# Optimization experiments

Measured on AMD Instinct MI355X. Metric: run time of the kernel, lower is better.

## Reference

```python
import jax, jax.numpy as jnp
import numpy as np

A_DIM = 12      # action dim (half of augmented state)
N_STEPS = 10    # Heun ODE steps (Flow.N)
P = 0.95        # mixing coefficient in _Heun_method


def _mlp(x, obs, t, W1, b1, W2, b2, W3, b3, W4, b4):
    h = jnp.concatenate([x, obs, t], axis=-1)
    h = jnp.tanh(h @ W1 + b1)
    h = jnp.tanh(h @ W2 + b2)
    h = jnp.tanh(h @ W3 + b3)
    return h @ W4 + b4


def _heun(obs, x, params):
    # Flow._Heun_method: sequential Heun integration of the augmented state.
    z = x[..., :A_DIM]
    y = x[..., A_DIM:]
    dt = 1.0 / N_STEPS
    tshape = x.shape[:-1] + (1,)

    def step(carry, i):
        z, y = carry
        t = jnp.ones(tshape, x.dtype) * (i / N_STEPS)
        z_t = _mlp(y, obs, t, *params)
        z_in = z + z_t * dt
        y_t = _mlp(z_in, obs, t, *params)
        y_in = y + y_t * dt
        z_new = P * z_in + (1.0 - P) * y_in
        y_new = P * y_in + (1.0 - P) * z_new
        return (z_new, y_new), None

    (z, y), _ = jax.lax.scan(step, (z, y), jnp.arange(N_STEPS, dtype=x.dtype))
    return jnp.concatenate([z, y], axis=-1)


def setup_inputs() -> dict:
    key = jax.random.key(0)
    ks = jax.random.split(key, 8)
    B, OBS, H, A = 2048, 48, 256, A_DIM
    din = A + OBS + 1  # 61
    s = 0.05  # small init scale to keep tanh unsaturated
    return {
        "observations": jax.random.normal(ks[0], (B, OBS), jnp.float32),
        "action_aug_0": jax.random.normal(ks[1], (B, 2 * A), jnp.float32),
        "W1": s * jax.random.normal(ks[2], (din, H), jnp.float32),
        "b1": jnp.zeros((H,), jnp.float32),
        "W2": s * jax.random.normal(ks[3], (H, H), jnp.float32),
        "b2": jnp.zeros((H,), jnp.float32),
        "W3": s * jax.random.normal(ks[4], (H, H), jnp.float32),
        "b3": jnp.zeros((H,), jnp.float32),
        "W4": s * jax.random.normal(ks[5], (H, A), jnp.float32),
        "b4": jnp.zeros((A,), jnp.float32),
        "jac": 1,
    }


def reference(observations, action_aug_0, W1, b1, W2, b2, W3, b3, W4, b4, jac):
    params = (W1, b1, W2, b2, W3, b3, W4, b4)
    action_aug = _heun(observations, action_aug_0, params)
    d = action_aug_0.shape[-1]
    # Normal(0, I) log prob summed over dims
    log_probs = -0.5 * jnp.sum(action_aug_0 ** 2, axis=-1) - 0.5 * d * jnp.log(2.0 * jnp.pi)
    if jac:
        single = lambda o, x: _heun(o, x, params)  # per-sample (obs_dim,), (2a,)
        J = jax.vmap(jax.jacrev(single, argnums=1))(observations, action_aug_0)  # (B, 2a, 2a)
        _, logabsdet = jnp.linalg.slogdet(J)  # = log|det J|
        log_probs = log_probs - logabsdet
    return action_aug, log_probs
```

## Files before the change

kernel.cpp:

```cpp
#include <hip/hip_runtime.h>
#include <hip/hip_bf16.h>


typedef unsigned short ushort_t;
typedef float f32x4 __attribute__((ext_vector_type(4)));
typedef short s16x8 __attribute__((ext_vector_type(8)));
typedef int   i32x4 __attribute__((ext_vector_type(4)));

#define NB      2048
#define OBS_D   48
#define HDIM    256
#define ADIM    12
#define XDIM    24
#define NSTEPS  10
#define DT      0.1f
#define PP      0.95f

#define W1U 0
#define W2U 16384
#define W3U 81920
#define W4U 147456
#define N_FRAG 151552
#define FRAG_BLOCKS 592
#define LP_BLOCKS 8

#define LDS_W2   0
#define LDS_BUFA 131072
#define LDS_BUFB 139264
#define LDS_AIN  147456
#define LDS_Z    149504
#define LDS_Y    150528
#define LDS_ZI   151552
#define LDS_TOTAL 152576

__device__ __forceinline__ ushort_t f2bf(float f) {
  unsigned u = __builtin_bit_cast(unsigned, f);
  u += 0x7fffu + ((u >> 16) & 1u);
  return (ushort_t)(u >> 16);
}

__device__ __forceinline__ float tanh_fast(float x) {
  float e = __builtin_amdgcn_exp2f(x * 2.885390081777927f);
  return 1.f - 2.f * __builtin_amdgcn_rcpf(1.f + e);
}

__global__ void prep_kernel(const float* __restrict__ W1, const float* __restrict__ b1,
                            const float* __restrict__ W2, const float* __restrict__ W3,
                            const float* __restrict__ W4, const float* __restrict__ x0,
                            const int* __restrict__ jac, float* __restrict__ out,
                            ushort_t* __restrict__ ws) {
  int bid = blockIdx.x;
  int tid = threadIdx.x;
  if (bid < FRAG_BLOCKS) {
    int e = bid * 256 + tid;
    float val = 0.f;
    if (e < 16384) {
      int kt = e >> 13; int r = e & 8191;
      int nt = r >> 9, l = (r >> 3) & 63, j = r & 7;
      int k = kt * 32 + ((l >> 4) << 3) + j;
      int col = nt * 16 + (l & 15);
      val = (k < 61) ? W1[k * 256 + col] : ((k == 61) ? b1[col] : 0.f);
    } else if (e < 81920) {
      int e2 = e - 16384;
      int kt = e2 >> 13; int r = e2 & 8191;
      int nt = r >> 9, l = (r >> 3) & 63, j = r & 7;
      int k = kt * 32 + ((l >> 4) << 3) + j;
      int col = nt * 16 + (l & 15);
      val = W2[k * 256 + col];
    } else if (e < 147456) {
      int e2 = e - 81920;
      int kt = e2 >> 13; int r = e2 & 8191;
      int nt = r >> 9, l = (r >> 3) & 63, j = r & 7;
      int k = kt * 32 + ((l >> 4) << 3) + j;
      int col = nt * 16 + (l & 15);
      val = W3[k * 256 + col];
    } else {
      int e2 = e - 147456;
      int kt = e2 >> 9; int r = e2 & 511;
      int l = (r >> 3) & 63, j = r & 7;
      int k = kt * 32 + ((l >> 4) << 3) + j;
      int col = l & 15;
      val = (col < 12) ? W4[k * 12 + col] : 0.f;
    }
    ws[e] = f2bf(val);
  } else {
    int s = (bid - FRAG_BLOCKS) * 256 + tid;
    float acc = 0.f;
    #pragma unroll 4
    for (int j = 0; j < XDIM; ++j) { float v = x0[s * XDIM + j]; acc += v * v; }
    float C = (jac[0] != 0) ? -9.744134143900015f : -22.054524796912143f;
    out[NB * XDIM + s] = -0.5f * acc + C;
  }
}

__global__ __launch_bounds__(512, 2) void flow_main(
    const float* __restrict__ obs, const float* __restrict__ x0,
    const float* __restrict__ b2g, const float* __restrict__ b3g,
    const float* __restrict__ b4g, const ushort_t* __restrict__ ws,
    float* __restrict__ out) {
  extern __shared__ char lds[];
  const int tid  = threadIdx.x;
  const int lane = tid & 63;
  const int wv   = tid >> 6;
  const int g    = lane >> 4;
  const int ar   = lane & 15;
  const int row0 = blockIdx.x * 16;

  ((unsigned*)(lds + LDS_AIN))[tid] = 0u;

  {
    const i32x4* __restrict__ src = (const i32x4*)(ws + W2U);
    i32x4* dst = (i32x4*)(lds + LDS_W2);
    #pragma unroll
    for (int it = 0; it < 16; ++it) dst[it * 512 + tid] = src[it * 512 + tid];
  }
  __syncthreads();

  for (int idx = tid; idx < 16 * OBS_D; idx += 512) {
    int r = idx / OBS_D, o = idx - r * OBS_D;
    int k = 12 + o;
    float v = obs[(row0 + r) * OBS_D + o];
    int byt = (k * 2) ^ ((r & 7) << 4);
    *(ushort_t*)(lds + LDS_AIN + r * 128 + byt) = f2bf(v);
  }
  if (tid < 16) {
    int byt = (61 * 2) ^ ((tid & 7) << 4);
    *(ushort_t*)(lds + LDS_AIN + tid * 128 + byt) = (ushort_t)0x3F80;
  }
  if (tid < 192) {
    int r = tid / 12, d = tid - r * 12;
    float zv = x0[(row0 + r) * XDIM + d];
    float yv = x0[(row0 + r) * XDIM + 12 + d];
    ((float*)(lds + LDS_Z))[r * 16 + d] = zv;
    ((float*)(lds + LDS_Y))[r * 16 + d] = yv;
    int byt = (d * 2) ^ ((r & 7) << 4);
    *(ushort_t*)(lds + LDS_AIN + r * 128 + byt) = f2bf(yv);
  }

  s16x8 w1r[2][2], w3r[8][2], w4r;
  #pragma unroll
  for (int kt = 0; kt < 2; ++kt)
    #pragma unroll
    for (int n = 0; n < 2; ++n)
      w1r[kt][n] = *(const s16x8*)(ws + W1U + (((kt * 16) + (2 * wv + n)) * 64 + lane) * 8);
  #pragma unroll
  for (int kt = 0; kt < 8; ++kt)
    #pragma unroll
    for (int n = 0; n < 2; ++n)
      w3r[kt][n] = *(const s16x8*)(ws + W3U + (((kt * 16) + (2 * wv + n)) * 64 + lane) * 8);
  w4r = *(const s16x8*)(ws + W4U + (wv * 64 + lane) * 8);

  float b2r[2], b3r[2];
  #pragma unroll
  for (int n = 0; n < 2; ++n) {
    b2r[n] = b2g[(2 * wv + n) * 16 + ar];
    b3r[n] = b3g[(2 * wv + n) * 16 + ar];
  }
  float b4v = (ar < 12) ? b4g[ar] : 0.f;

  __syncthreads();

  const f32x4 z4 = {0.f, 0.f, 0.f, 0.f};

  for (int i = 0; i < NSTEPS; ++i) {
    #pragma unroll
    for (int ev = 0; ev < 2; ++ev) {
      f32x4 acc0 = z4, acc1 = z4;
      #pragma unroll
      for (int kt = 0; kt < 2; ++kt) {
        int off = kt * 64 + g * 16;
        s16x8 a = *(const s16x8*)(lds + LDS_AIN + ar * 128 + (off ^ ((ar & 7) << 4)));
        acc0 = __builtin_amdgcn_mfma_f32_16x16x32_bf16(a, w1r[kt][0], acc0, 0, 0, 0);
        acc1 = __builtin_amdgcn_mfma_f32_16x16x32_bf16(a, w1r[kt][1], acc1, 0, 0, 0);
      }
      #pragma unroll
      for (int n = 0; n < 2; ++n) {
        f32x4 acc = n ? acc1 : acc0;
        int colg = (2 * wv + n) * 16 + ar;
        #pragma unroll
        for (int r = 0; r < 4; ++r) {
          int rw = g * 4 + r;
          float h = tanh_fast(acc[r]);
          int byt = (colg * 2) ^ ((rw & 7) << 4);
          *(ushort_t*)(lds + LDS_BUFA + rw * 512 + byt) = f2bf(h);
        }
      }
      __syncthreads();

      acc0 = z4; acc1 = z4;
      #pragma unroll
      for (int kt = 0; kt < 8; ++kt) {
        int off = kt * 64 + g * 16;
        s16x8 a = *(const s16x8*)(lds + LDS_BUFA + ar * 512 + (off ^ ((ar & 7) << 4)));
        s16x8 bb0 = *(const s16x8*)(lds + LDS_W2 + (((kt * 16) + (2 * wv)) * 64 + lane) * 16);
        s16x8 bb1 = *(const s16x8*)(lds + LDS_W2 + (((kt * 16) + (2 * wv + 1)) * 64 + lane) * 16);
        acc0 = __builtin_amdgcn_mfma_f32_16x16x32_bf16(a, bb0, acc0, 0, 0, 0);
        acc1 = __builtin_amdgcn_mfma_f32_16x16x32_bf16(a, bb1, acc1, 0, 0, 0);
      }
      #pragma unroll
      for (int n = 0; n < 2; ++n) {
        f32x4 acc = n ? acc1 : acc0;
        int colg = (2 * wv + n) * 16 + ar;
        #pragma unroll
        for (int r = 0; r < 4; ++r) {
          int rw = g * 4 + r;
          float h = tanh_fast(acc[r] + b2r[n]);
          int byt = (colg * 2) ^ ((rw & 7) << 4);
          *(ushort_t*)(lds + LDS_BUFB + rw * 512 + byt) = f2bf(h);
        }
      }
      __syncthreads();

      acc0 = z4; acc1 = z4;
      #pragma unroll
      for (int kt = 0; kt < 8; ++kt) {
        int off = kt * 64 + g * 16;
        s16x8 a = *(const s16x8*)(lds + LDS_BUFB + ar * 512 + (off ^ ((ar & 7) << 4)));
        acc0 = __builtin_amdgcn_mfma_f32_16x16x32_bf16(a, w3r[kt][0], acc0, 0, 0, 0);
        acc1 = __builtin_amdgcn_mfma_f32_16x16x32_bf16(a, w3r[kt][1], acc1, 0, 0, 0);
      }
      #pragma unroll
      for (int n = 0; n < 2; ++n) {
        f32x4 acc = n ? acc1 : acc0;
        int colg = (2 * wv + n) * 16 + ar;
        #pragma unroll
        for (int r = 0; r < 4; ++r) {
          int rw = g * 4 + r;
          float h = tanh_fast(acc[r] + b3r[n]);
          int byt = (colg * 2) ^ ((rw & 7) << 4);
          *(ushort_t*)(lds + LDS_BUFA + rw * 512 + byt) = f2bf(h);
        }
      }
      __syncthreads();

      {
        int off = wv * 64 + g * 16;
        s16x8 a = *(const s16x8*)(lds + LDS_BUFA + ar * 512 + (off ^ ((ar & 7) << 4)));
        f32x4 p = __builtin_amdgcn_mfma_f32_16x16x32_bf16(a, w4r, z4, 0, 0, 0);
        #pragma unroll
        for (int r = 0; r < 4; ++r) {
          int rw = g * 4 + r;
          *(float*)(lds + LDS_BUFB + wv * 1024 + (rw * 16 + ar) * 4) = p[r];
        }
      }
      __syncthreads();

      if (tid < 256) {
        float s = b4v;
        #pragma unroll
        for (int w = 0; w < 8; ++w) s += *(const float*)(lds + LDS_BUFB + w * 1024 + tid * 4);
        int r = tid >> 4, c = tid & 15;
        if (c < 12) {
          int byt = (c * 2) ^ ((r & 7) << 4);
          if (ev == 0) {
            float zi = ((float*)(lds + LDS_Z))[tid] + DT * s;
            ((float*)(lds + LDS_ZI))[tid] = zi;
            *(ushort_t*)(lds + LDS_AIN + r * 128 + byt) = f2bf(zi);
          } else {
            float yi = ((float*)(lds + LDS_Y))[tid] + DT * s;
            float zi = ((float*)(lds + LDS_ZI))[tid];
            float zn = PP * zi + (1.f - PP) * yi;
            float yn = PP * yi + (1.f - PP) * zn;
            ((float*)(lds + LDS_Z))[tid] = zn;
            ((float*)(lds + LDS_Y))[tid] = yn;
            *(ushort_t*)(lds + LDS_AIN + r * 128 + byt) = f2bf(yn);
          }
        }
        if (ev == 1 && c == 15) {
          float tn = (float)(i + 1) * DT;
          int byt = (60 * 2) ^ ((r & 7) << 4);
          *(ushort_t*)(lds + LDS_AIN + r * 128 + byt) = f2bf(tn);
        }
      }
      __syncthreads();
    }
  }

  if (tid < 256) {
    int r = tid >> 4, c = tid & 15;
    if (c < 12) {
      out[(row0 + r) * XDIM + c]      = ((float*)(lds + LDS_Z))[tid];
      out[(row0 + r) * XDIM + 12 + c] = ((float*)(lds + LDS_Y))[tid];
    }
  }
}

extern "C" void kernel_launch(void* const* d_in, const int* in_sizes, int n_in,
                              void* d_out, int out_size, void* d_ws, size_t ws_size,
                              hipStream_t stream) {
  const float* obs = (const float*)d_in[0];
  const float* x0  = (const float*)d_in[1];
  const float* W1  = (const float*)d_in[2];
  const float* b1  = (const float*)d_in[3];
  const float* W2  = (const float*)d_in[4];
  const float* b2  = (const float*)d_in[5];
  const float* W3  = (const float*)d_in[6];
  const float* b3  = (const float*)d_in[7];
  const float* W4  = (const float*)d_in[8];
  const float* b4  = (const float*)d_in[9];
  const int*   jac = (const int*)d_in[10];
  float* out = (float*)d_out;
  ushort_t* ws = (ushort_t*)d_ws;

  hipFuncSetAttribute((const void*)flow_main,
                      hipFuncAttributeMaxDynamicSharedMemorySize, LDS_TOTAL);

  prep_kernel<<<FRAG_BLOCKS + LP_BLOCKS, 256, 0, stream>>>(W1, b1, W2, W3, W4, x0, jac, out, ws);
  flow_main<<<128, 512, LDS_TOTAL, stream>>>(obs, x0, b2, b3, b4, ws, out);
}
```

Baseline: 56.55 us.

## Keep W2 in registers, repack LDS activation layout, drop a barrier

W2 fragments are now held in registers like W3 instead of being staged in a 128KB LDS buffer, which removes the LDS copy at kernel start and the per-step W2 LDS reads. The weight fragment K ordering and the activation LDS layout are permuted so each lane writes packed 32-bit pairs with padded row strides instead of XOR-swizzled 16-bit stores. The barrier before the final layer is replaced by a local lgkmcnt wait, since each wave reads only the columns it wrote itself. z/y state is kept in registers instead of LDS. The cost is much higher register pressure, which may spill under launch_bounds(512,2).

```diff
diff --git a/kernel.cpp b/kernel.cpp
--- a/kernel.cpp
+++ b/kernel.cpp
@@ -5,7 +5,6 @@
 typedef unsigned short ushort_t;
 typedef float f32x4 __attribute__((ext_vector_type(4)));
 typedef short s16x8 __attribute__((ext_vector_type(8)));
-typedef int   i32x4 __attribute__((ext_vector_type(4)));
 
 #define NB      2048
 #define OBS_D   48
@@ -24,14 +23,11 @@
 #define FRAG_BLOCKS 592
 #define LP_BLOCKS 8
 
-#define LDS_W2   0
-#define LDS_BUFA 131072
-#define LDS_BUFB 139264
-#define LDS_AIN  147456
-#define LDS_Z    149504
-#define LDS_Y    150528
-#define LDS_ZI   151552
-#define LDS_TOTAL 152576
+#define LDS_BUFA 0
+#define LDS_BUFB 9216
+#define LDS_AIN  18432
+#define LDS_PART 21504
+#define LDS_TOTAL 31744
 
 __device__ __forceinline__ ushort_t f2bf(float f) {
   unsigned u = __builtin_bit_cast(unsigned, f);
@@ -42,6 +38,10 @@
 __device__ __forceinline__ float tanh_fast(float x) {
   float e = __builtin_amdgcn_exp2f(x * 2.885390081777927f);
   return 1.f - 2.f * __builtin_amdgcn_rcpf(1.f + e);
+}
+
+__device__ __forceinline__ int ain_byte(int r, int c) {
+  return r * 192 + ((c >> 5) << 6) + ((c & 15) << 2) + (((c >> 4) & 1) << 1);
 }
 
 __global__ void prep_kernel(const float* __restrict__ W1, const float* __restrict__ b1,
@@ -57,28 +57,28 @@
     if (e < 16384) {
       int kt = e >> 13; int r = e & 8191;
       int nt = r >> 9, l = (r >> 3) & 63, j = r & 7;
-      int k = kt * 32 + ((l >> 4) << 3) + j;
+      int k = kt * 32 + ((l >> 4) << 2) + (j >> 1) + ((j & 1) << 4);
       int col = nt * 16 + (l & 15);
       val = (k < 61) ? W1[k * 256 + col] : ((k == 61) ? b1[col] : 0.f);
     } else if (e < 81920) {
       int e2 = e - 16384;
       int kt = e2 >> 13; int r = e2 & 8191;
       int nt = r >> 9, l = (r >> 3) & 63, j = r & 7;
-      int k = kt * 32 + ((l >> 4) << 3) + j;
+      int k = kt * 32 + ((l >> 4) << 2) + (j >> 1) + ((j & 1) << 4);
       int col = nt * 16 + (l & 15);
       val = W2[k * 256 + col];
     } else if (e < 147456) {
       int e2 = e - 81920;
       int kt = e2 >> 13; int r = e2 & 8191;
       int nt = r >> 9, l = (r >> 3) & 63, j = r & 7;
-      int k = kt * 32 + ((l >> 4) << 3) + j;
+      int k = kt * 32 + ((l >> 4) << 2) + (j >> 1) + ((j & 1) << 4);
       int col = nt * 16 + (l & 15);
       val = W3[k * 256 + col];
     } else {
       int e2 = e - 147456;
       int kt = e2 >> 9; int r = e2 & 511;
       int l = (r >> 3) & 63, j = r & 7;
-      int k = kt * 32 + ((l >> 4) << 3) + j;
+      int k = kt * 32 + ((l >> 4) << 2) + (j >> 1) + ((j & 1) << 4);
       int col = l & 15;
       val = (col < 12) ? W4[k * 12 + col] : 0.f;
     }
@@ -98,7 +98,7 @@
     const float* __restrict__ b2g, const float* __restrict__ b3g,
     const float* __restrict__ b4g, const ushort_t* __restrict__ ws,
     float* __restrict__ out) {
-  extern __shared__ char lds[];
+  __shared__ char lds[LDS_TOTAL];
   const int tid  = threadIdx.x;
   const int lane = tid & 63;
   const int wv   = tid >> 6;
@@ -106,38 +106,30 @@
   const int ar   = lane & 15;
   const int row0 = blockIdx.x * 16;
 
-  ((unsigned*)(lds + LDS_AIN))[tid] = 0u;
-
-  {
-    const i32x4* __restrict__ src = (const i32x4*)(ws + W2U);
-    i32x4* dst = (i32x4*)(lds + LDS_W2);
-    #pragma unroll
-    for (int it = 0; it < 16; ++it) dst[it * 512 + tid] = src[it * 512 + tid];
-  }
+  const int aA = LDS_AIN + ar * 192 + g * 16;
+  const int hA = ar * 576 + (((ar >> 2) & 1) << 6) + g * 16;
+  const int hw = (g * 4) * 576 + ((g & 1) << 6) + wv * 64 + ar * 4;
+  const int pw = LDS_PART + wv * 1280 + (g * 4) * 80 + ar * 4;
+  const int rs = tid >> 4, cs = tid & 15;
+
+  for (int p = tid; p < 768; p += 512) ((unsigned*)(lds + LDS_AIN))[p] = 0u;
   __syncthreads();
 
   for (int idx = tid; idx < 16 * OBS_D; idx += 512) {
     int r = idx / OBS_D, o = idx - r * OBS_D;
-    int k = 12 + o;
-    float v = obs[(row0 + r) * OBS_D + o];
-    int byt = (k * 2) ^ ((r & 7) << 4);
-    *(ushort_t*)(lds + LDS_AIN + r * 128 + byt) = f2bf(v);
-  }
-  if (tid < 16) {
-    int byt = (61 * 2) ^ ((tid & 7) << 4);
-    *(ushort_t*)(lds + LDS_AIN + tid * 128 + byt) = (ushort_t)0x3F80;
-  }
-  if (tid < 192) {
-    int r = tid / 12, d = tid - r * 12;
-    float zv = x0[(row0 + r) * XDIM + d];
-    float yv = x0[(row0 + r) * XDIM + 12 + d];
-    ((float*)(lds + LDS_Z))[r * 16 + d] = zv;
-    ((float*)(lds + LDS_Y))[r * 16 + d] = yv;
-    int byt = (d * 2) ^ ((r & 7) << 4);
-    *(ushort_t*)(lds + LDS_AIN + r * 128 + byt) = f2bf(yv);
-  }
-
-  s16x8 w1r[2][2], w3r[8][2], w4r;
+    *(ushort_t*)(lds + LDS_AIN + ain_byte(r, 12 + o)) = f2bf(obs[(row0 + r) * OBS_D + o]);
+  }
+  if (tid < 16)
+    *(ushort_t*)(lds + LDS_AIN + tid * 192 + 118) = (ushort_t)0x3F80;
+
+  float zr = 0.f, yr = 0.f, zir = 0.f;
+  if (tid < 256 && cs < 12) {
+    zr = x0[(row0 + rs) * XDIM + cs];
+    yr = x0[(row0 + rs) * XDIM + 12 + cs];
+    *(ushort_t*)(lds + LDS_AIN + rs * 192 + cs * 4) = f2bf(yr);
+  }
+
+  s16x8 w1r[2][2], w2r[8][2], w3r[8][2], w4r;
   #pragma unroll
   for (int kt = 0; kt < 2; ++kt)
     #pragma unroll
@@ -146,8 +138,10 @@
   #pragma unroll
   for (int kt = 0; kt < 8; ++kt)
     #pragma unroll
-    for (int n = 0; n < 2; ++n)
+    for (int n = 0; n < 2; ++n) {
+      w2r[kt][n] = *(const s16x8*)(ws + W2U + (((kt * 16) + (2 * wv + n)) * 64 + lane) * 8);
       w3r[kt][n] = *(const s16x8*)(ws + W3U + (((kt * 16) + (2 * wv + n)) * 64 + lane) * 8);
+    }
   w4r = *(const s16x8*)(ws + W4U + (wv * 64 + lane) * 8);
 
   float b2r[2], b3r[2];
@@ -156,7 +150,7 @@
     b2r[n] = b2g[(2 * wv + n) * 16 + ar];
     b3r[n] = b3g[(2 * wv + n) * 16 + ar];
   }
-  float b4v = (ar < 12) ? b4g[ar] : 0.f;
+  const float b4v = (cs < 12) ? b4g[cs] : 0.f;
 
   __syncthreads();
 
@@ -168,120 +162,84 @@
       f32x4 acc0 = z4, acc1 = z4;
       #pragma unroll
       for (int kt = 0; kt < 2; ++kt) {
-        int off = kt * 64 + g * 16;
-        s16x8 a = *(const s16x8*)(lds + LDS_AIN + ar * 128 + (off ^ ((ar & 7) << 4)));
+        s16x8 a = *(const s16x8*)(lds + aA + kt * 64);
         acc0 = __builtin_amdgcn_mfma_f32_16x16x32_bf16(a, w1r[kt][0], acc0, 0, 0, 0);
         acc1 = __builtin_amdgcn_mfma_f32_16x16x32_bf16(a, w1r[kt][1], acc1, 0, 0, 0);
       }
       #pragma unroll
-      for (int n = 0; n < 2; ++n) {
-        f32x4 acc = n ? acc1 : acc0;
-        int colg = (2 * wv + n) * 16 + ar;
-        #pragma unroll
-        for (int r = 0; r < 4; ++r) {
-          int rw = g * 4 + r;
-          float h = tanh_fast(acc[r]);
-          int byt = (colg * 2) ^ ((rw & 7) << 4);
-          *(ushort_t*)(lds + LDS_BUFA + rw * 512 + byt) = f2bf(h);
-        }
+      for (int r = 0; r < 4; ++r) {
+        unsigned p = (unsigned)f2bf(tanh_fast(acc0[r]))
+                   | ((unsigned)f2bf(tanh_fast(acc1[r])) << 16);
+        *(unsigned*)(lds + LDS_BUFA + hw + r * 576) = p;
       }
       __syncthreads();
 
       acc0 = z4; acc1 = z4;
       #pragma unroll
       for (int kt = 0; kt < 8; ++kt) {
-        int off = kt * 64 + g * 16;
-        s16x8 a = *(const s16x8*)(lds + LDS_BUFA + ar * 512 + (off ^ ((ar & 7) << 4)));
-        s16x8 bb0 = *(const s16x8*)(lds + LDS_W2 + (((kt * 16) + (2 * wv)) * 64 + lane) * 16);
-        s16x8 bb1 = *(const s16x8*)(lds + LDS_W2 + (((kt * 16) + (2 * wv + 1)) * 64 + lane) * 16);
-        acc0 = __builtin_amdgcn_mfma_f32_16x16x32_bf16(a, bb0, acc0, 0, 0, 0);
-        acc1 = __builtin_amdgcn_mfma_f32_16x16x32_bf16(a, bb1, acc1, 0, 0, 0);
-      }
-      #pragma unroll
-      for (int n = 0; n < 2; ++n) {
-        f32x4 acc = n ? acc1 : acc0;
-        int colg = (2 * wv + n) * 16 + ar;
-        #pragma unroll
-        for (int r = 0; r < 4; ++r) {
-          int rw = g * 4 + r;
-          float h = tanh_fast(acc[r] + b2r[n]);
-          int byt = (colg * 2) ^ ((rw & 7) << 4);
-          *(ushort_t*)(lds + LDS_BUFB + rw * 512 + byt) = f2bf(h);
-        }
+        s16x8 a = *(const s16x8*)(lds + LDS_BUFA + hA + kt * 64);
+        acc0 = __builtin_amdgcn_mfma_f32_16x16x32_bf16(a, w2r[kt][0], acc0, 0, 0, 0);
+        acc1 = __builtin_amdgcn_mfma_f32_16x16x32_bf16(a, w2r[kt][1], acc1, 0, 0, 0);
+      }
+      #pragma unroll
+      for (int r = 0; r < 4; ++r) {
+        unsigned p = (unsigned)f2bf(tanh_fast(acc0[r] + b2r[0]))
+                   | ((unsigned)f2bf(tanh_fast(acc1[r] + b2r[1])) << 16);
+        *(unsigned*)(lds + LDS_BUFB + hw + r * 576) = p;
       }
       __syncthreads();
 
       acc0 = z4; acc1 = z4;
       #pragma unroll
       for (int kt = 0; kt < 8; ++kt) {
-        int off = kt * 64 + g * 16;
-        s16x8 a = *(const s16x8*)(lds + LDS_BUFB + ar * 512 + (off ^ ((ar & 7) << 4)));
+        s16x8 a = *(const s16x8*)(lds + LDS_BUFB + hA + kt * 64);
         acc0 = __builtin_amdgcn_mfma_f32_16x16x32_bf16(a, w3r[kt][0], acc0, 0, 0, 0);
         acc1 = __builtin_amdgcn_mfma_f32_16x16x32_bf16(a, w3r[kt][1], acc1, 0, 0, 0);
       }
       #pragma unroll
-      for (int n = 0; n < 2; ++n) {
-        f32x4 acc = n ? acc1 : acc0;
-        int colg = (2 * wv + n) * 16 + ar;
+      for (int r = 0; r < 4; ++r) {
+        unsigned p = (unsigned)f2bf(tanh_fast(acc0[r] + b3r[0]))
+                   | ((unsigned)f2bf(tanh_fast(acc1[r] + b3r[1])) << 16);
+        *(unsigned*)(lds + LDS_BUFA + hw + r * 576) = p;
+      }
+
+      asm volatile("s_waitcnt lgkmcnt(0)" ::: "memory");
+      __builtin_amdgcn_sched_barrier(0);
+      {
+        s16x8 a = *(const s16x8*)(lds + LDS_BUFA + hA + wv * 64);
+        f32x4 p4 = __builtin_amdgcn_mfma_f32_16x16x32_bf16(a, w4r, z4, 0, 0, 0);
         #pragma unroll
-        for (int r = 0; r < 4; ++r) {
-          int rw = g * 4 + r;
-          float h = tanh_fast(acc[r] + b3r[n]);
-          int byt = (colg * 2) ^ ((rw & 7) << 4);
-          *(ushort_t*)(lds + LDS_BUFA + rw * 512 + byt) = f2bf(h);
-        }
-      }
-      __syncthreads();
-
-      {
-        int off = wv * 64 + g * 16;
-        s16x8 a = *(const s16x8*)(lds + LDS_BUFA + ar * 512 + (off ^ ((ar & 7) << 4)));
-        f32x4 p = __builtin_amdgcn_mfma_f32_16x16x32_bf16(a, w4r, z4, 0, 0, 0);
-        #pragma unroll
-        for (int r = 0; r < 4; ++r) {
-          int rw = g * 4 + r;
-          *(float*)(lds + LDS_BUFB + wv * 1024 + (rw * 16 + ar) * 4) = p[r];
-        }
+        for (int r = 0; r < 4; ++r)
+          *(float*)(lds + pw + r * 80) = p4[r];
       }
       __syncthreads();
 
       if (tid < 256) {
         float s = b4v;
         #pragma unroll
-        for (int w = 0; w < 8; ++w) s += *(const float*)(lds + LDS_BUFB + w * 1024 + tid * 4);
-        int r = tid >> 4, c = tid & 15;
-        if (c < 12) {
-          int byt = (c * 2) ^ ((r & 7) << 4);
+        for (int w = 0; w < 8; ++w)
+          s += *(const float*)(lds + LDS_PART + w * 1280 + rs * 80 + cs * 4);
+        if (cs < 12) {
           if (ev == 0) {
-            float zi = ((float*)(lds + LDS_Z))[tid] + DT * s;
-            ((float*)(lds + LDS_ZI))[tid] = zi;
-            *(ushort_t*)(lds + LDS_AIN + r * 128 + byt) = f2bf(zi);
+            zir = zr + DT * s;
+            *(ushort_t*)(lds + LDS_AIN + rs * 192 + cs * 4) = f2bf(zir);
           } else {
-            float yi = ((float*)(lds + LDS_Y))[tid] + DT * s;
-            float zi = ((float*)(lds + LDS_ZI))[tid];
-            float zn = PP * zi + (1.f - PP) * yi;
-            float yn = PP * yi + (1.f - PP) * zn;
-            ((float*)(lds + LDS_Z))[tid] = zn;
-            ((float*)(lds + LDS_Y))[tid] = yn;
-            *(ushort_t*)(lds + LDS_AIN + r * 128 + byt) = f2bf(yn);
+            float yi = yr + DT * s;
+            zr = PP * zir + (1.f - PP) * yi;
+            yr = PP * yi + (1.f - PP) * zr;
+            *(ushort_t*)(lds + LDS_AIN + rs * 192 + cs * 4) = f2bf(yr);
           }
         }
-        if (ev == 1 && c == 15) {
-          float tn = (float)(i + 1) * DT;
-          int byt = (60 * 2) ^ ((r & 7) << 4);
-          *(ushort_t*)(lds + LDS_AIN + r * 128 + byt) = f2bf(tn);
-        }
+        if (ev == 1 && cs == 15)
+          *(ushort_t*)(lds + LDS_AIN + rs * 192 + 114) = f2bf((float)(i + 1) * DT);
       }
       __syncthreads();
     }
   }
 
-  if (tid < 256) {
-    int r = tid >> 4, c = tid & 15;
-    if (c < 12) {
-      out[(row0 + r) * XDIM + c]      = ((float*)(lds + LDS_Z))[tid];
-      out[(row0 + r) * XDIM + 12 + c] = ((float*)(lds + LDS_Y))[tid];
-    }
+  if (tid < 256 && cs < 12) {
+    out[(row0 + rs) * XDIM + cs]      = zr;
+    out[(row0 + rs) * XDIM + 12 + cs] = yr;
   }
 }
 
@@ -302,9 +260,6 @@
   float* out = (float*)d_out;
   ushort_t* ws = (ushort_t*)d_ws;
 
-  hipFuncSetAttribute((const void*)flow_main,
-                      hipFuncAttributeMaxDynamicSharedMemorySize, LDS_TOTAL);
-
   prep_kernel<<<FRAG_BLOCKS + LP_BLOCKS, 256, 0, stream>>>(W1, b1, W2, W3, W4, x0, jac, out, ws);
-  flow_main<<<128, 512, LDS_TOTAL, stream>>>(obs, x0, b2, b3, b4, ws, out);
-}
+  flow_main<<<128, 512, 0, stream>>>(obs, x0, b2, b3, b4, ws, out);
+}
```

Result: faster. 49.71 us (-12.1%).
